# Performance work log

Measured on AMD Instinct MI355X. Metric: run time of the kernel, lower is better.

## Reference

```python
import jax, jax.numpy as jnp
import numpy as np

OBS_DIM = 32
STATE_DIM = 5
LSTM_H = 64
T_HID = 128
O_HID = 128
B = 128
T = 2048


def _xavier(key, shape):
    fan_out, fan_in = shape
    std = (2.0 / (fan_in + fan_out)) ** 0.5
    return jax.random.normal(key, shape, dtype=jnp.float32) * std


def setup_inputs() -> dict:
    key = jax.random.key(0)
    ks = jax.random.split(key, 16)
    inp = {}
    inp["observations"] = jax.random.normal(ks[0], (B, T, OBS_DIM), dtype=jnp.float32)
    # LSTM params (PyTorch layout: [4H, in], gate order i,f,g,o)
    inp["lstm_Wih"] = _xavier(ks[1], (4 * LSTM_H, OBS_DIM))
    inp["lstm_Whh"] = _xavier(ks[2], (4 * LSTM_H, LSTM_H))
    inp["lstm_bih"] = jnp.zeros((4 * LSTM_H,), dtype=jnp.float32)
    inp["lstm_bhh"] = jnp.zeros((4 * LSTM_H,), dtype=jnp.float32)
    # transition MLP
    inp["t_w1"] = _xavier(ks[3], (T_HID, LSTM_H + STATE_DIM))
    inp["t_b1"] = jnp.zeros((T_HID,), dtype=jnp.float32)
    inp["t_g"] = jnp.ones((T_HID,), dtype=jnp.float32)
    inp["t_beta"] = jnp.zeros((T_HID,), dtype=jnp.float32)
    inp["t_w2"] = _xavier(ks[4], (T_HID // 2, T_HID))
    inp["t_b2"] = jnp.zeros((T_HID // 2,), dtype=jnp.float32)
    inp["t_w3"] = _xavier(ks[5], (2 * STATE_DIM, T_HID // 2))
    inp["t_b3"] = jnp.zeros((2 * STATE_DIM,), dtype=jnp.float32)
    # observation MLP
    inp["o_w1"] = _xavier(ks[6], (O_HID, STATE_DIM))
    inp["o_b1"] = jnp.zeros((O_HID,), dtype=jnp.float32)
    inp["o_g"] = jnp.ones((O_HID,), dtype=jnp.float32)
    inp["o_beta"] = jnp.zeros((O_HID,), dtype=jnp.float32)
    inp["o_w2"] = _xavier(ks[7], (O_HID // 2, O_HID))
    inp["o_b2"] = jnp.zeros((O_HID // 2,), dtype=jnp.float32)
    inp["o_w3"] = _xavier(ks[8], (2 * OBS_DIM, O_HID // 2))
    inp["o_b3"] = jnp.zeros((2 * OBS_DIM,), dtype=jnp.float32)
    inp["z0_mean"] = jnp.zeros((STATE_DIM,), dtype=jnp.float32)
    inp["z0_log_var"] = jnp.zeros((STATE_DIM,), dtype=jnp.float32)
    return inp


def _layernorm(x, g, b, eps=1e-5):
    m = jnp.mean(x, axis=-1, keepdims=True)
    v = jnp.mean((x - m) ** 2, axis=-1, keepdims=True)
    return (x - m) * jax.lax.rsqrt(v + eps) * g + b


def _forward(observations, lstm_Wih, lstm_Whh, lstm_bih, lstm_bhh,
             t_w1, t_b1, t_g, t_beta, t_w2, t_b2, t_w3, t_b3,
             o_w1, o_b1, o_g, o_beta, o_w2, o_b2, o_w3, o_b3,
             z0_mean, z0_log_var):
    b, s, _ = observations.shape
    # ---- LSTM (batch_first); precompute input projection, scan over time ----
    x_proj = jnp.einsum("bti,gi->btg", observations, lstm_Wih) + lstm_bih + lstm_bhh  # [B,T,4H]
    x_proj = jnp.swapaxes(x_proj, 0, 1)  # [T,B,4H]

    def lstm_step(carry, xt):
        h, c = carry
        gates = xt + h @ lstm_Whh.T
        i, f, g, o = jnp.split(gates, 4, axis=-1)
        i = jax.nn.sigmoid(i); f = jax.nn.sigmoid(f)
        g = jnp.tanh(g); o = jax.nn.sigmoid(o)
        c = f * c + i * g
        h = o * jnp.tanh(c)
        return (h, c), h

    h0 = jnp.zeros((b, LSTM_H), dtype=observations.dtype)
    c0 = jnp.zeros((b, LSTM_H), dtype=observations.dtype)
    _, lstm_seq = jax.lax.scan(lstm_step, (h0, c0), x_proj)  # [T,B,H]

    # ---- state-space recurrence (eval mode: z = transition mean) ----
    z0 = jnp.broadcast_to(z0_mean, (b, STATE_DIM))

    def trans_step(z, lstm_t):
        comb = jnp.concatenate([lstm_t, z], axis=-1)            # [B, H+S]
        h1 = jnp.tanh(_layernorm(comb @ t_w1.T + t_b1, t_g, t_beta))
        h2 = jnp.tanh(h1 @ t_w2.T + t_b2)
        out = h2 @ t_w3.T + t_b3                                 # [B, 2S]
        mean = out[..., :STATE_DIM]
        log_var = jnp.clip(out[..., STATE_DIM:], -10.0, 10.0)
        return mean, (mean, log_var)

    _, (t_means, t_lvs) = jax.lax.scan(trans_step, z0, lstm_seq[1:])  # [T-1,B,S]

    trans_means = jnp.concatenate([z0[None], t_means], axis=0)                              # [T,B,S]
    trans_log_vars = jnp.concatenate([jnp.broadcast_to(z0_log_var, (1, b, STATE_DIM)), t_lvs], axis=0)
    states = trans_means  # eval mode: z_t == trans_mean_t, z_0 == z0_mean

    # ---- observation head, vectorized over all timesteps ----
    h1 = jnp.tanh(_layernorm(states @ o_w1.T + o_b1, o_g, o_beta))
    h2 = jnp.tanh(h1 @ o_w2.T + o_b2)
    out = h2 @ o_w3.T + o_b3                                      # [T,B,2*obs_dim]
    obs_means = out[..., :OBS_DIM]
    obs_log_vars = jnp.clip(out[..., OBS_DIM:], -10.0, 10.0)

    # move to batch_first [B,T,*]
    return (jnp.swapaxes(obs_means, 0, 1),
            jnp.swapaxes(obs_log_vars, 0, 1),
            jnp.swapaxes(trans_means, 0, 1),
            jnp.swapaxes(trans_log_vars, 0, 1))


def reference(observations, lstm_Wih, lstm_Whh, lstm_bih, lstm_bhh,
              t_w1, t_b1, t_g, t_beta, t_w2, t_b2, t_w3, t_b3,
              o_w1, o_b1, o_g, o_beta, o_w2, o_b2, o_w3, o_b3,
              z0_mean, z0_log_var):
    return _forward(observations, lstm_Wih, lstm_Whh, lstm_bih, lstm_bhh,
                    t_w1, t_b1, t_g, t_beta, t_w2, t_b2, t_w3, t_b3,
                    o_w1, o_b1, o_g, o_beta, o_w2, o_b2, o_w3, o_b3,
                    z0_mean, z0_log_var)
```

## Files before the change

kernel.cpp:

```cpp
#include <hip/hip_runtime.h>

#define B_ 128
#define T_ 2048

typedef float vf32 __attribute__((ext_vector_type(32)));

__device__ __forceinline__ float fast_sigmoid(float x){
    return 1.0f / (1.0f + __expf(-x));
}
__device__ __forceinline__ float fast_tanh(float x){
    float a = fabsf(x);
    float e = __expf(2.0f*a);
    float r = 1.0f - 2.0f/(e + 1.0f);
    return (x < 0.0f) ? -r : r;
}

__device__ __forceinline__ void wait_ge(int* p, int v){
    while (__hip_atomic_load(p, __ATOMIC_ACQUIRE, __HIP_MEMORY_SCOPE_WORKGROUP) < v) { }
}
__device__ __forceinline__ void st_rel(int* p, int v){
    __hip_atomic_store(p, v, __ATOMIC_RELEASE, __HIP_MEMORY_SCOPE_WORKGROUP);
}

__global__ __launch_bounds__(512)
__attribute__((amdgpu_waves_per_eu(2, 2)))
void scan_kernel(
    const float* __restrict__ obs,
    const float* __restrict__ Wih,
    const float* __restrict__ Whh,
    const float* __restrict__ bih,
    const float* __restrict__ bhh,
    const float* __restrict__ tw1,
    const float* __restrict__ tb1,
    const float* __restrict__ tg,
    const float* __restrict__ tbeta,
    const float* __restrict__ tw2,
    const float* __restrict__ tb2,
    const float* __restrict__ tw3,
    const float* __restrict__ tb3,
    const float* __restrict__ z0m,
    const float* __restrict__ z0lv,
    float* __restrict__ out_tm,
    float* __restrict__ out_tlv)
{
    __shared__ __align__(16) float hring[8][64];
    __shared__ __align__(16) float oring[8][32];
    __shared__ __align__(16) float A1ring[8][128];
    __shared__ __align__(16) float h1w[2][64];
    __shared__ float p2s[64];
    __shared__ float z_s[8];
    __shared__ int hflag[4];
    __shared__ int aflag[2];
    __shared__ int p2flag;
    __shared__ int ttag;

    const int tid  = threadIdx.x;
    const int wid  = tid >> 6;
    const int lane = tid & 63;
    const int b    = blockIdx.x;

    vf32 V0, V1, V2;
    #pragma unroll
    for (int k = 0; k < 32; k++) { V0[k]=0.f; V1[k]=0.f; V2[k]=0.f; }

    float biasg = 0.f, b1r = 0.f, gr = 0.f, betar = 0.f, b2r = 0.f, b3r = 0.f;
    float c_st = 0.f, carry = 0.f;

    if (wid < 4) {
        const int g  = lane & 3;
        const int uu = wid*16 + (lane >> 2);
        const int row = g*64 + uu;
        biasg = bih[row] + bhh[row];
        #pragma unroll
        for (int k = 0; k < 32; k++) V0[k] = Wih[row*32 + k];
        #pragma unroll
        for (int k = 0; k < 32; k++) V1[k] = Whh[row*64 + k];
        #pragma unroll
        for (int k = 0; k < 32; k++) V2[k] = Whh[row*64 + 32 + k];
        if (g == 1 && uu < 32) carry = obs[((size_t)b*T_ + 4)*32 + uu];
    } else if (wid < 6) {
        const int ks = wid - 4;
        #pragma unroll
        for (int k = 0; k < 32; k++) V0[k] = tw2[lane*128 + ks*64 + k];
        #pragma unroll
        for (int k = 0; k < 32; k++) V1[k] = tw2[lane*128 + ks*64 + 32 + k];
        #pragma unroll
        for (int k = 0; k < 5; k++) {
            V2[k]     = tw1[lane*69 + 64 + k];
            V2[5 + k] = tw1[(64 + lane)*69 + 64 + k];
        }
        const int r = ks*64 + lane;
        gr = tg[r]; betar = tbeta[r];
        if (ks == 0) {
            b2r = tb2[lane];
            if (lane < 40) {
                #pragma unroll
                for (int k = 0; k < 16; k++)
                    V2[10 + k] = tw3[(lane>>2)*64 + (lane&3)*16 + k];
                b3r = tb3[lane >> 2];
            }
        }
    } else {
        const int r = (wid - 6)*64 + lane;
        #pragma unroll
        for (int k = 0; k < 32; k++) V0[k] = tw1[r*69 + k];
        #pragma unroll
        for (int k = 0; k < 32; k++) V1[k] = tw1[r*69 + 32 + k];
        b1r = tb1[r];
    }

    if (tid < 64) hring[7][tid] = 0.f;
    if (tid < 128) oring[tid >> 5][tid & 31] = obs[(size_t)b*T_*32 + tid];
    if (tid < 5) {
        z_s[tid] = z0m[tid];
        out_tm [(size_t)b*T_*5 + tid] = z0m[tid];
        out_tlv[(size_t)b*T_*5 + tid] = z0lv[tid];
    }
    if (tid < 4) hflag[tid] = -1;
    if (tid < 2) aflag[tid] = 0;
    if (tid == 0) { p2flag = 0; ttag = 0; }
    __syncthreads();

    if (wid < 4) {
        const int g  = lane & 3;
        const int uu = wid*16 + (lane >> 2);
        for (int t = 0; t < T_; ++t) {
            wait_ge(&hflag[0], t-1); wait_ge(&hflag[1], t-1);
            wait_ge(&hflag[2], t-1); wait_ge(&hflag[3], t-1);
            wait_ge(&aflag[0], t-8); wait_ge(&aflag[1], t-8);

            const float4* ob = (const float4*)oring[t & 7];
            const float4* hp = (const float4*)hring[(t - 1) & 7];
            float a0 = biasg, a1 = 0.f, a2 = 0.f, a3 = 0.f;
            #pragma unroll
            for (int k4 = 0; k4 < 8; k4++) {
                float4 o = ob[k4];
                a0 += V0[k4*4+0]*o.x;
                a1 += V0[k4*4+1]*o.y;
                a2 += V0[k4*4+2]*o.z;
                a3 += V0[k4*4+3]*o.w;
            }
            #pragma unroll
            for (int k4 = 0; k4 < 8; k4++) {
                float4 h = hp[k4];
                a0 += V1[k4*4+0]*h.x;
                a1 += V1[k4*4+1]*h.y;
                a2 += V1[k4*4+2]*h.z;
                a3 += V1[k4*4+3]*h.w;
            }
            #pragma unroll
            for (int k4 = 0; k4 < 8; k4++) {
                float4 h = hp[8 + k4];
                a0 += V2[k4*4+0]*h.x;
                a1 += V2[k4*4+1]*h.y;
                a2 += V2[k4*4+2]*h.z;
                a3 += V2[k4*4+3]*h.w;
            }
            const float G = (a0 + a1) + (a2 + a3);

            const float x1 = __shfl_xor(G, 1, 64);
            const float x2 = __shfl_xor(G, 2, 64);
            const float x3 = __shfl_xor(x1, 2, 64);
            const bool c1 = (g & 1), c2 = (g & 2);
            float iv = c2 ? (c1 ? x3 : x2) : (c1 ? x1 : G );
            float fv = c2 ? (c1 ? x2 : x3) : (c1 ? G  : x1);
            float gv = c2 ? (c1 ? x1 : G ) : (c1 ? x3 : x2);
            float ov = c2 ? (c1 ? G  : x1) : (c1 ? x2 : x3);

            iv = fast_sigmoid(iv);
            fv = fast_sigmoid(fv);
            gv = fast_tanh(gv);
            ov = fast_sigmoid(ov);
            c_st = fv*c_st + iv*gv;
            const float hv = ov * fast_tanh(c_st);

            if (g == 0) hring[t & 7][uu] = hv;
            if (g == 1 && uu < 32 && t + 4 < T_) oring[(t + 4) & 7][uu] = carry;
            st_rel(&hflag[wid], t);
            if (g == 1 && uu < 32 && t + 5 < T_)
                carry = obs[((size_t)b*T_ + t + 5)*32 + uu];
        }
    } else if (wid < 6) {
        const int ks = wid - 4;
        for (int t = 1; t < T_; ++t) {
            wait_ge(&aflag[0], t); wait_ge(&aflag[1], t);
            wait_ge(&ttag, t - 1);

            const float z0 = z_s[0], z1 = z_s[1], z2 = z_s[2],
                        z3 = z_s[3], z4 = z_s[4];
            float a0 = A1ring[t & 7][lane]
                     + V2[0]*z0 + V2[1]*z1 + V2[2]*z2 + V2[3]*z3 + V2[4]*z4;
            float a1 = A1ring[t & 7][64 + lane]
                     + V2[5]*z0 + V2[6]*z1 + V2[7]*z2 + V2[8]*z3 + V2[9]*z4;
            float s1 = a0 + a1, s2 = a0*a0 + a1*a1;
            #pragma unroll
            for (int m = 1; m < 64; m <<= 1) {
                s1 += __shfl_xor(s1, m, 64);
                s2 += __shfl_xor(s2, m, 64);
            }
            const float mean = s1 * (1.0f/128.0f);
            const float ms   = s2 * (1.0f/128.0f);
            const float var  = fmaxf(ms - mean*mean, 0.0f);
            const float rs   = rsqrtf(var + 1e-5f);
            const float aown = ks ? a1 : a0;
            const float h1v  = fast_tanh((aown - mean)*rs*gr + betar);

            h1w[ks][lane] = h1v;
            __builtin_amdgcn_wave_barrier();

            float p0 = 0.f, p1 = 0.f, p2 = 0.f, p3 = 0.f;
            const float4* h4 = (const float4*)h1w[ks];
            #pragma unroll
            for (int k4 = 0; k4 < 8; k4++) {
                float4 h = h4[k4];
                p0 += V0[k4*4+0]*h.x;
                p1 += V0[k4*4+1]*h.y;
                p2 += V0[k4*4+2]*h.z;
                p3 += V0[k4*4+3]*h.w;
            }
            #pragma unroll
            for (int k4 = 0; k4 < 8; k4++) {
                float4 h = h4[8 + k4];
                p0 += V1[k4*4+0]*h.x;
                p1 += V1[k4*4+1]*h.y;
                p2 += V1[k4*4+2]*h.z;
                p3 += V1[k4*4+3]*h.w;
            }
            const float p = (p0 + p1) + (p2 + p3);

            if (ks == 1) {
                p2s[lane] = p;
                st_rel(&p2flag, t);
            } else {
                wait_ge(&p2flag, t);
                const float h2v = fast_tanh(b2r + p + p2s[lane]);
                const int pp = lane & 3;
                float acc = 0.f;
                #pragma unroll
                for (int k = 0; k < 16; k++)
                    acc += V2[10 + k] * __shfl(h2v, pp*16 + k, 64);
                acc += __shfl_xor(acc, 1, 64);
                acc += __shfl_xor(acc, 2, 64);
                if (pp == 0 && lane < 40) {
                    const int j = lane >> 2;
                    const float val = b3r + acc;
                    const size_t row = (size_t)b*T_ + t;
                    if (j < 5) {
                        z_s[j] = val;
                        out_tm[row*5 + j] = val;
                    } else {
                        out_tlv[row*5 + (j - 5)] = fminf(10.0f, fmaxf(-10.0f, val));
                    }
                }
                st_rel(&ttag, t);
            }
        }
    } else {
        const int r = (wid - 6)*64 + lane;
        for (int t = 1; t < T_; ++t) {
            wait_ge(&hflag[0], t); wait_ge(&hflag[1], t);
            wait_ge(&hflag[2], t); wait_ge(&hflag[3], t);
            wait_ge(&ttag, t - 8);

            const float4* hv4 = (const float4*)hring[t & 7];
            float s0 = b1r, s1 = 0.f, s2 = 0.f, s3 = 0.f;
            #pragma unroll
            for (int k4 = 0; k4 < 8; k4++) {
                float4 h = hv4[k4];
                s0 += V0[k4*4+0]*h.x;
                s1 += V0[k4*4+1]*h.y;
                s2 += V0[k4*4+2]*h.z;
                s3 += V0[k4*4+3]*h.w;
            }
            #pragma unroll
            for (int k4 = 0; k4 < 8; k4++) {
                float4 h = hv4[8 + k4];
                s0 += V1[k4*4+0]*h.x;
                s1 += V1[k4*4+1]*h.y;
                s2 += V1[k4*4+2]*h.z;
                s3 += V1[k4*4+3]*h.w;
            }
            A1ring[t & 7][r] = (s0 + s1) + (s2 + s3);
            st_rel(&aflag[wid - 6], t);
        }
    }
}

#define DEC_BLOCKS 512

__global__ __launch_bounds__(512) void dec_kernel(
    const float* __restrict__ ow1,
    const float* __restrict__ ob1,
    const float* __restrict__ og,
    const float* __restrict__ obeta,
    const float* __restrict__ ow2,
    const float* __restrict__ ob2,
    const float* __restrict__ ow3,
    const float* __restrict__ ob3,
    const float* __restrict__ tmeans,
    float* __restrict__ out_om,
    float* __restrict__ out_olv)
{
    __shared__ float w1s[640];
    __shared__ float b1s[128], gs[128], bes[128];
    __shared__ float w2s[8192];
    __shared__ float b2s[64];
    __shared__ float w3s[4096];
    __shared__ float b3s[64];
    __shared__ __align__(16) float h1s[8][128];
    __shared__ __align__(16) float h2s[8][64];

    const int tid = threadIdx.x;
    for (int idx = tid; idx < 640; idx += 512) w1s[idx] = ow1[idx];
    for (int idx = tid; idx < 128; idx += 512) {
        b1s[idx] = ob1[idx]; gs[idx] = og[idx]; bes[idx] = obeta[idx];
    }
    for (int idx = tid; idx < 8192; idx += 512) {
        int k = idx >> 6, j = idx & 63;
        w2s[idx] = ow2[j*128 + k];
    }
    for (int idx = tid; idx < 4096; idx += 512) {
        int k = idx >> 6, j = idx & 63;
        w3s[idx] = ow3[j*64 + k];
    }
    for (int idx = tid; idx < 64; idx += 512) { b2s[idx] = ob2[idx]; b3s[idx] = ob3[idx]; }
    __syncthreads();

    const int lane   = tid & 63;
    const int wv     = tid >> 6;
    const int gwave  = (blockIdx.x * 512 + tid) >> 6;
    const int nwaves = DEC_BLOCKS * 8;
    const int j0 = lane, j1 = lane + 64;

    for (int row = gwave; row < B_*T_; row += nwaves) {
        const float z0v = tmeans[(size_t)row*5 + 0];
        const float z1v = tmeans[(size_t)row*5 + 1];
        const float z2v = tmeans[(size_t)row*5 + 2];
        const float z3v = tmeans[(size_t)row*5 + 3];
        const float z4v = tmeans[(size_t)row*5 + 4];

        float a = b1s[j0] + w1s[j0*5+0]*z0v + w1s[j0*5+1]*z1v + w1s[j0*5+2]*z2v
                + w1s[j0*5+3]*z3v + w1s[j0*5+4]*z4v;
        float bb = b1s[j1] + w1s[j1*5+0]*z0v + w1s[j1*5+1]*z1v + w1s[j1*5+2]*z2v
                 + w1s[j1*5+3]*z3v + w1s[j1*5+4]*z4v;
        float s1 = a + bb, s2 = a*a + bb*bb;
        #pragma unroll
        for (int m = 1; m < 64; m <<= 1) {
            s1 += __shfl_xor(s1, m, 64);
            s2 += __shfl_xor(s2, m, 64);
        }
        const float mean = s1 * (1.0f/128.0f);
        const float var  = fmaxf(s2 * (1.0f/128.0f) - mean*mean, 0.0f);
        const float rs   = rsqrtf(var + 1e-5f);
        const float h1a  = fast_tanh((a  - mean)*rs*gs[j0] + bes[j0]);
        const float h1b  = fast_tanh((bb - mean)*rs*gs[j1] + bes[j1]);

        h1s[wv][lane]      = h1a;
        h1s[wv][64 + lane] = h1b;
        __builtin_amdgcn_wave_barrier();

        float acc2a = b2s[lane], acc2b = 0.f, acc2c = 0.f, acc2d = 0.f;
        const float4* h14 = (const float4*)(h1s[wv]);
        #pragma unroll
        for (int k4 = 0; k4 < 32; k4++) {
            float4 h = h14[k4];
            acc2a += h.x * w2s[(k4*4+0)*64 + lane];
            acc2b += h.y * w2s[(k4*4+1)*64 + lane];
            acc2c += h.z * w2s[(k4*4+2)*64 + lane];
            acc2d += h.w * w2s[(k4*4+3)*64 + lane];
        }
        const float h2v = fast_tanh(acc2a + acc2b + acc2c + acc2d);

        h2s[wv][lane] = h2v;
        __builtin_amdgcn_wave_barrier();

        float acc3a = b3s[lane], acc3b = 0.f, acc3c = 0.f, acc3d = 0.f;
        const float4* h24 = (const float4*)(h2s[wv]);
        #pragma unroll
        for (int k4 = 0; k4 < 16; k4++) {
            float4 h = h24[k4];
            acc3a += h.x * w3s[(k4*4+0)*64 + lane];
            acc3b += h.y * w3s[(k4*4+1)*64 + lane];
            acc3c += h.z * w3s[(k4*4+2)*64 + lane];
            acc3d += h.w * w3s[(k4*4+3)*64 + lane];
        }
        const float acc3 = acc3a + acc3b + acc3c + acc3d;

        if (lane < 32) {
            out_om[(size_t)row*32 + lane] = acc3;
        } else {
            out_olv[(size_t)row*32 + (lane - 32)] = fminf(10.0f, fmaxf(-10.0f, acc3));
        }
    }
}

extern "C" void kernel_launch(void* const* d_in, const int* in_sizes, int n_in,
                              void* d_out, int out_size, void* d_ws, size_t ws_size,
                              hipStream_t stream) {
    const float* obs  = (const float*)d_in[0];
    const float* Wih  = (const float*)d_in[1];
    const float* Whh  = (const float*)d_in[2];
    const float* bih  = (const float*)d_in[3];
    const float* bhh  = (const float*)d_in[4];
    const float* tw1  = (const float*)d_in[5];
    const float* tb1  = (const float*)d_in[6];
    const float* tg   = (const float*)d_in[7];
    const float* tbe  = (const float*)d_in[8];
    const float* tw2  = (const float*)d_in[9];
    const float* tb2  = (const float*)d_in[10];
    const float* tw3  = (const float*)d_in[11];
    const float* tb3  = (const float*)d_in[12];
    const float* ow1  = (const float*)d_in[13];
    const float* ob1  = (const float*)d_in[14];
    const float* og   = (const float*)d_in[15];
    const float* obe  = (const float*)d_in[16];
    const float* ow2  = (const float*)d_in[17];
    const float* ob2  = (const float*)d_in[18];
    const float* ow3  = (const float*)d_in[19];
    const float* ob3  = (const float*)d_in[20];
    const float* z0m  = (const float*)d_in[21];
    const float* z0lv = (const float*)d_in[22];

    float* out0 = (float*)d_out;
    float* out1 = out0 + (size_t)B_*T_*32;
    float* out2 = out1 + (size_t)B_*T_*32;
    float* out3 = out2 + (size_t)B_*T_*5;

    scan_kernel<<<B_, 512, 0, stream>>>(obs, Wih, Whh, bih, bhh,
                                        tw1, tb1, tg, tbe, tw2, tb2, tw3, tb3,
                                        z0m, z0lv, out2, out3);

    dec_kernel<<<DEC_BLOCKS, 512, 0, stream>>>(
        ow1, ob1, og, obe, ow2, ob2, ow3, ob3, out2, out0, out1);
}
```

Before: 3.136 ms.

## Replicate transition output layer in both MLP waves and use DPP reductions

Both transition-MLP waves now exchange their partial layer-2 sums symmetrically through a double-buffered shared array and each computes the final output layer redundantly. This lets each wave keep the next state z in registers via shuffles, dropping the shared z_s round trip and the wait on ttag in the critical serial chain. Wave-wide sums and the gate quad exchange now use DPP moves and permlane swaps instead of ds_bpermute shuffles, cutting latency per step. It adds duplicate FLOPs in the second wave and relies on the DPP control codes being correct for the reduction patterns.

```diff
diff --git a/kernel.cpp b/kernel.cpp
--- a/kernel.cpp
+++ b/kernel.cpp
@@ -13,6 +13,38 @@
     float e = __expf(2.0f*a);
     float r = 1.0f - 2.0f/(e + 1.0f);
     return (x < 0.0f) ? -r : r;
+}
+
+template<int CTRL>
+__device__ __forceinline__ float dpp_mov(float x){
+    return __int_as_float(__builtin_amdgcn_update_dpp(
+        0, __float_as_int(x), CTRL, 0xF, 0xF, true));
+}
+
+__device__ __forceinline__ float wave_sum64(float v){
+    v += dpp_mov<0xB1>(v);
+    v += dpp_mov<0x4E>(v);
+    v += dpp_mov<0x141>(v);
+    v += dpp_mov<0x140>(v);
+#if __has_builtin(__builtin_amdgcn_permlane16_swap)
+    {
+        auto r = __builtin_amdgcn_permlane16_swap(__float_as_int(v),
+                                                  __float_as_int(v), false, false);
+        v = __int_as_float(r[0]) + __int_as_float(r[1]);
+    }
+#else
+    v += __shfl_xor(v, 16, 64);
+#endif
+#if __has_builtin(__builtin_amdgcn_permlane32_swap)
+    {
+        auto r = __builtin_amdgcn_permlane32_swap(__float_as_int(v),
+                                                  __float_as_int(v), false, false);
+        v = __int_as_float(r[0]) + __int_as_float(r[1]);
+    }
+#else
+    v += __shfl_xor(v, 32, 64);
+#endif
+    return v;
 }
 
 __device__ __forceinline__ void wait_ge(int* p, int v){
@@ -47,11 +79,10 @@
     __shared__ __align__(16) float oring[8][32];
     __shared__ __align__(16) float A1ring[8][128];
     __shared__ __align__(16) float h1w[2][64];
-    __shared__ float p2s[64];
-    __shared__ float z_s[8];
+    __shared__ float p2s[2][2][64];
     __shared__ int hflag[4];
     __shared__ int aflag[2];
-    __shared__ int p2flag;
+    __shared__ int pf[2];
     __shared__ int ttag;
 
     const int tid  = threadIdx.x;
@@ -91,14 +122,12 @@
         }
         const int r = ks*64 + lane;
         gr = tg[r]; betar = tbeta[r];
-        if (ks == 0) {
-            b2r = tb2[lane];
-            if (lane < 40) {
-                #pragma unroll
-                for (int k = 0; k < 16; k++)
-                    V2[10 + k] = tw3[(lane>>2)*64 + (lane&3)*16 + k];
-                b3r = tb3[lane >> 2];
-            }
+        b2r = tb2[lane];
+        if (lane < 40) {
+            #pragma unroll
+            for (int k = 0; k < 16; k++)
+                V2[10 + k] = tw3[(lane>>2)*64 + (lane&3)*16 + k];
+            b3r = tb3[lane >> 2];
         }
     } else {
         const int r = (wid - 6)*64 + lane;
@@ -112,13 +141,12 @@
     if (tid < 64) hring[7][tid] = 0.f;
     if (tid < 128) oring[tid >> 5][tid & 31] = obs[(size_t)b*T_*32 + tid];
     if (tid < 5) {
-        z_s[tid] = z0m[tid];
         out_tm [(size_t)b*T_*5 + tid] = z0m[tid];
         out_tlv[(size_t)b*T_*5 + tid] = z0lv[tid];
     }
     if (tid < 4) hflag[tid] = -1;
-    if (tid < 2) aflag[tid] = 0;
-    if (tid == 0) { p2flag = 0; ttag = 0; }
+    if (tid < 2) { aflag[tid] = 0; pf[tid] = 0; }
+    if (tid == 0) ttag = 0;
     __syncthreads();
 
     if (wid < 4) {
@@ -158,9 +186,9 @@
             }
             const float G = (a0 + a1) + (a2 + a3);
 
-            const float x1 = __shfl_xor(G, 1, 64);
-            const float x2 = __shfl_xor(G, 2, 64);
-            const float x3 = __shfl_xor(x1, 2, 64);
+            const float x1 = dpp_mov<0xB1>(G);
+            const float x2 = dpp_mov<0x4E>(G);
+            const float x3 = dpp_mov<0x1B>(G);
             const bool c1 = (g & 1), c2 = (g & 2);
             float iv = c2 ? (c1 ? x3 : x2) : (c1 ? x1 : G );
             float fv = c2 ? (c1 ? x2 : x3) : (c1 ? G  : x1);
@@ -182,25 +210,19 @@
         }
     } else if (wid < 6) {
         const int ks = wid - 4;
+        float zr0 = z0m[0], zr1 = z0m[1], zr2 = z0m[2],
+              zr3 = z0m[3], zr4 = z0m[4];
         for (int t = 1; t < T_; ++t) {
             wait_ge(&aflag[0], t); wait_ge(&aflag[1], t);
-            wait_ge(&ttag, t - 1);
-
-            const float z0 = z_s[0], z1 = z_s[1], z2 = z_s[2],
-                        z3 = z_s[3], z4 = z_s[4];
+
             float a0 = A1ring[t & 7][lane]
-                     + V2[0]*z0 + V2[1]*z1 + V2[2]*z2 + V2[3]*z3 + V2[4]*z4;
+                     + V2[0]*zr0 + V2[1]*zr1 + V2[2]*zr2 + V2[3]*zr3 + V2[4]*zr4;
             float a1 = A1ring[t & 7][64 + lane]
-                     + V2[5]*z0 + V2[6]*z1 + V2[7]*z2 + V2[8]*z3 + V2[9]*z4;
-            float s1 = a0 + a1, s2 = a0*a0 + a1*a1;
-            #pragma unroll
-            for (int m = 1; m < 64; m <<= 1) {
-                s1 += __shfl_xor(s1, m, 64);
-                s2 += __shfl_xor(s2, m, 64);
-            }
+                     + V2[5]*zr0 + V2[6]*zr1 + V2[7]*zr2 + V2[8]*zr3 + V2[9]*zr4;
+            const float s1 = wave_sum64(a0 + a1);
+            const float s2 = wave_sum64(a0*a0 + a1*a1);
             const float mean = s1 * (1.0f/128.0f);
-            const float ms   = s2 * (1.0f/128.0f);
-            const float var  = fmaxf(ms - mean*mean, 0.0f);
+            const float var  = fmaxf(s2 * (1.0f/128.0f) - mean*mean, 0.0f);
             const float rs   = rsqrtf(var + 1e-5f);
             const float aown = ks ? a1 : a0;
             const float h1v  = fast_tanh((aown - mean)*rs*gr + betar);
@@ -228,32 +250,41 @@
             }
             const float p = (p0 + p1) + (p2 + p3);
 
-            if (ks == 1) {
-                p2s[lane] = p;
-                st_rel(&p2flag, t);
-            } else {
-                wait_ge(&p2flag, t);
-                const float h2v = fast_tanh(b2r + p + p2s[lane]);
-                const int pp = lane & 3;
-                float acc = 0.f;
-                #pragma unroll
-                for (int k = 0; k < 16; k++)
-                    acc += V2[10 + k] * __shfl(h2v, pp*16 + k, 64);
-                acc += __shfl_xor(acc, 1, 64);
-                acc += __shfl_xor(acc, 2, 64);
+            p2s[t & 1][ks][lane] = p;
+            st_rel(&pf[ks], t);
+            wait_ge(&pf[ks ^ 1], t);
+            const float pother = p2s[t & 1][ks ^ 1][lane];
+
+            const float h2v = fast_tanh(b2r + p + pother);
+            const int pp = lane & 3;
+            float ac0 = 0.f, ac1 = 0.f, ac2 = 0.f, ac3 = 0.f;
+            #pragma unroll
+            for (int k = 0; k < 4; k++) {
+                ac0 += V2[10 + k]      * __shfl(h2v, pp*16 + k,      64);
+                ac1 += V2[10 + 4 + k]  * __shfl(h2v, pp*16 + 4 + k,  64);
+                ac2 += V2[10 + 8 + k]  * __shfl(h2v, pp*16 + 8 + k,  64);
+                ac3 += V2[10 + 12 + k] * __shfl(h2v, pp*16 + 12 + k, 64);
+            }
+            float acc = (ac0 + ac1) + (ac2 + ac3);
+            acc += dpp_mov<0xB1>(acc);
+            acc += dpp_mov<0x4E>(acc);
+            const float val = b3r + acc;
+
+            if (ks == 0) {
                 if (pp == 0 && lane < 40) {
                     const int j = lane >> 2;
-                    const float val = b3r + acc;
                     const size_t row = (size_t)b*T_ + t;
-                    if (j < 5) {
-                        z_s[j] = val;
-                        out_tm[row*5 + j] = val;
-                    } else {
-                        out_tlv[row*5 + (j - 5)] = fminf(10.0f, fmaxf(-10.0f, val));
-                    }
+                    if (j < 5) out_tm[row*5 + j] = val;
+                    else out_tlv[row*5 + (j - 5)] =
+                             fminf(10.0f, fmaxf(-10.0f, val));
                 }
                 st_rel(&ttag, t);
             }
+            zr0 = __shfl(val, 0, 64);
+            zr1 = __shfl(val, 4, 64);
+            zr2 = __shfl(val, 8, 64);
+            zr3 = __shfl(val, 12, 64);
+            zr4 = __shfl(val, 16, 64);
         }
     } else {
         const int r = (wid - 6)*64 + lane;
@@ -343,12 +374,8 @@
                 + w1s[j0*5+3]*z3v + w1s[j0*5+4]*z4v;
         float bb = b1s[j1] + w1s[j1*5+0]*z0v + w1s[j1*5+1]*z1v + w1s[j1*5+2]*z2v
                  + w1s[j1*5+3]*z3v + w1s[j1*5+4]*z4v;
-        float s1 = a + bb, s2 = a*a + bb*bb;
-        #pragma unroll
-        for (int m = 1; m < 64; m <<= 1) {
-            s1 += __shfl_xor(s1, m, 64);
-            s2 += __shfl_xor(s2, m, 64);
-        }
+        const float s1 = wave_sum64(a + bb);
+        const float s2 = wave_sum64(a*a + bb*bb);
         const float mean = s1 * (1.0f/128.0f);
         const float var  = fmaxf(s2 * (1.0f/128.0f) - mean*mean, 0.0f);
         const float rs   = rsqrtf(var + 1e-5f);
```

Measured after the change: 2.759 ms. -12.0%, faster.
